# Kernel tuning notes

Measured on AMD Instinct MI355X. Metric: run time of the kernel, lower is better.

Reference implementation:

```python
import jax, jax.numpy as jnp
import numpy as np

B, S, N, H, C = 64, 512, 24, 768, 6

CONST_LAST = jnp.array([0.1, 0.1, 0.1, 0.3, 0.8, 0.01], dtype=jnp.float32)
CONST_MID = jnp.array([0.1, 0.1, 0.1, 0.8, 0.3, 0.01], dtype=jnp.float32)


def setup_inputs() -> dict:
    key = jax.random.key(0)
    k1, k2, k3, k4 = jax.random.split(key, 4)
    last_hidden_state = jax.random.normal(k1, (B, S, H), dtype=jnp.float32)
    # strictly increasing boundaries in [0, S-1]: sort randint in [0, S-N) then add arange(N)
    base = jnp.sort(jax.random.randint(k2, (B, N), 0, S - N), axis=1)
    sentence_token = base + jnp.arange(N, dtype=base.dtype)[None, :]
    W = jax.random.normal(k3, (C, H), dtype=jnp.float32) * 0.02
    b = jax.random.normal(k4, (C,), dtype=jnp.float32) * 0.02
    return {"last_hidden_state": last_hidden_state, "sentence_token": sentence_token,
            "W": W, "b": b}


def reference(last_hidden_state, sentence_token, W, b):
    # last_hidden_state: [B,S,H]; sentence_token: [B,N] strictly increasing boundaries.
    # Segment j covers tokens [prev+1, t_j] inclusive (prev = -1 for j==0).
    ends = sentence_token                                            # [B,N]
    prev = jnp.concatenate([-jnp.ones_like(ends[:, :1]), ends[:, :-1]], axis=1)
    # prefix sums with leading zero: csp[:, t+1] = sum of tokens 0..t
    cs = jnp.cumsum(last_hidden_state, axis=1)                       # [B,S,H]
    csp = jnp.concatenate([jnp.zeros_like(cs[:, :1]), cs], axis=1)   # [B,S+1,H]
    seg_sum = (jnp.take_along_axis(csp, (ends + 1)[:, :, None], axis=1)
               - jnp.take_along_axis(csp, (prev + 1)[:, :, None], axis=1))  # [B,N,H]
    lens = (ends - prev).astype(last_hidden_state.dtype)[:, :, None]  # >= 1 by construction
    seg_mean = seg_sum / lens                                         # [B,N,H]
    probs = jax.nn.sigmoid(jnp.einsum('bnh,ch->bnc', seg_mean, W) + b)  # [B,N,C]
    # override: boundary > 500 -> constant probability vector (different if last sentence)
    is_last = (jnp.arange(ends.shape[1]) == ends.shape[1] - 1)[None, :, None]  # [1,N,1]
    const = jnp.where(is_last, CONST_LAST[None, None, :], CONST_MID[None, None, :])
    over = (ends > 500)[:, :, None]
    return jnp.where(over, const, probs)
```

## Files before the change

### kernel.cpp

```cpp
#include <hip/hip_runtime.h>
#include <math.h>

#define B_ 64
#define S_ 512
#define N_ 24
#define H_ 768
#define C_ 6

__global__ __launch_bounds__(256) void proj_seg_kernel(
    const float* __restrict__ lhs, const int* __restrict__ st,
    const float* __restrict__ W, float* __restrict__ segsum, int ntok) {
  const int lane = threadIdx.x & 63;
  const int gwave = (int)((blockIdx.x * blockDim.x + threadIdx.x) >> 6);
  const int nwaves = (int)((gridDim.x * blockDim.x) >> 6);

  const float4* W4 = (const float4*)W;
  float4 w[3][C_];
#pragma unroll
  for (int k = 0; k < 3; ++k)
#pragma unroll
    for (int c = 0; c < C_; ++c)
      w[k][c] = W4[c * (H_ / 4) + k * 64 + lane];

  for (int t = gwave; t < ntok; t += nwaves) {
    const int b = t >> 9;
    const int s = t & 511;
    const int* stb = st + b * N_;
    if (s > stb[N_ - 1]) continue;

    int lo = 0, hi = N_ - 1;
    while (lo < hi) {
      int mid = (lo + hi) >> 1;
      if (stb[mid] < s) lo = mid + 1; else hi = mid;
    }

    const float4* x4 = (const float4*)(lhs + (size_t)t * H_);
    float acc[C_];
#pragma unroll
    for (int c = 0; c < C_; ++c) acc[c] = 0.0f;
#pragma unroll
    for (int k = 0; k < 3; ++k) {
      float4 x = x4[k * 64 + lane];
#pragma unroll
      for (int c = 0; c < C_; ++c)
        acc[c] += x.x * w[k][c].x + x.y * w[k][c].y +
                  x.z * w[k][c].z + x.w * w[k][c].w;
    }
#pragma unroll
    for (int c = 0; c < C_; ++c) {
      float v = acc[c];
      v += __shfl_down(v, 32, 64);
      v += __shfl_down(v, 16, 64);
      v += __shfl_down(v, 8, 64);
      v += __shfl_down(v, 4, 64);
      v += __shfl_down(v, 2, 64);
      v += __shfl_down(v, 1, 64);
      acc[c] = v;
    }
    if (lane == 0) {
      float* dst = segsum + ((size_t)b * N_ + lo) * C_;
#pragma unroll
      for (int c = 0; c < C_; ++c) atomicAdd(dst + c, acc[c]);
    }
  }
}

__global__ __launch_bounds__(256) void finalize_kernel(
    const float* __restrict__ segsum, const int* __restrict__ st,
    const float* __restrict__ bias, float* __restrict__ out) {
  int idx = blockIdx.x * blockDim.x + threadIdx.x;
  if (idx >= B_ * N_ * C_) return;
  int c = idx % C_;
  int j = (idx / C_) % N_;
  int b = idx / (N_ * C_);
  int end = st[b * N_ + j];
  int prev = (j == 0) ? -1 : st[b * N_ + j - 1];
  float len = (float)(end - prev);
  float logit = segsum[idx] / len + bias[c];
  float p = 1.0f / (1.0f + expf(-logit));
  if (end > 500) {
    float cl = (c < 3) ? 0.1f : (c == 3 ? 0.3f : (c == 4 ? 0.8f : 0.01f));
    float cm = (c < 3) ? 0.1f : (c == 3 ? 0.8f : (c == 4 ? 0.3f : 0.01f));
    p = (j == N_ - 1) ? cl : cm;
  }
  out[idx] = p;
}

extern "C" void kernel_launch(void* const* d_in, const int* in_sizes, int n_in,
                              void* d_out, int out_size, void* d_ws, size_t ws_size,
                              hipStream_t stream) {
  const float* lhs  = (const float*)d_in[0];
  const int*   st   = (const int*)d_in[1];
  const float* W    = (const float*)d_in[2];
  const float* bias = (const float*)d_in[3];
  float* segsum = (float*)d_ws;

  hipMemsetAsync(d_ws, 0, (size_t)B_ * N_ * C_ * sizeof(float), stream);
  proj_seg_kernel<<<2048, 256, 0, stream>>>(lhs, st, W, segsum, B_ * S_);
  finalize_kernel<<<(B_ * N_ * C_ + 255) / 256, 256, 0, stream>>>(
      segsum, st, bias, (float*)d_out);
}
```

Baseline: 183.7 us.

## Restructure segment projection into per-block LDS accumulators with chunked token tiles

Each block now owns a contiguous chunk of tokens for one batch and accumulates per-lane partial projections into a shared-memory array indexed by segment, class and lane. This replaces the per-token 6x6 shuffle reductions and global atomics. Segment lookup becomes a ballot/popcount over the boundaries held in registers instead of a binary search. Per-chunk partials go to workspace and are summed in the finalize kernel, with a fallback to global atomics when the workspace is too small. The costs are 36KB of LDS per block, LDS atomics, and extra finalize reads.

```diff
diff --git a/kernel.cpp b/kernel.cpp
--- a/kernel.cpp
+++ b/kernel.cpp
@@ -6,13 +6,40 @@
 #define N_ 24
 #define H_ 768
 #define C_ 6
+#define CHUNKS 16
+#define TOK_PER_BLOCK (S_ / CHUNKS)
+#define TOK_PER_WAVE (TOK_PER_BLOCK/4)
 
-__global__ __launch_bounds__(256) void proj_seg_kernel(
+__device__ __forceinline__ void do_token(const float4 x[3], const float4 w[3][C_],
+                                         int seg, int lane, float* acc) {
+  float a[C_];
+#pragma unroll
+  for (int c = 0; c < C_; ++c) a[c] = 0.f;
+#pragma unroll
+  for (int k = 0; k < 3; ++k)
+#pragma unroll
+    for (int c = 0; c < C_; ++c)
+      a[c] += x[k].x * w[k][c].x + x[k].y * w[k][c].y +
+              x[k].z * w[k][c].z + x[k].w * w[k][c].w;
+#pragma unroll
+  for (int c = 0; c < C_; ++c)
+    atomicAdd(&acc[(seg * C_ + c) * 64 + lane], a[c]);
+}
+
+__global__ __launch_bounds__(256, 4) void seg_proj_kernel(
     const float* __restrict__ lhs, const int* __restrict__ st,
-    const float* __restrict__ W, float* __restrict__ segsum, int ntok) {
-  const int lane = threadIdx.x & 63;
-  const int gwave = (int)((blockIdx.x * blockDim.x + threadIdx.x) >> 6);
-  const int nwaves = (int)((gridDim.x * blockDim.x) >> 6);
+    const float* __restrict__ W, float* __restrict__ outbuf, int use_atomic) {
+  __shared__ float acc[N_ * C_ * 64];
+  const int tid = threadIdx.x;
+  const int lane = tid & 63;
+  const int wave = tid >> 6;
+  const int b = blockIdx.x / CHUNKS;
+  const int chunk = blockIdx.x % CHUNKS;
+
+  for (int i = tid; i < N_ * C_ * 64; i += 256) acc[i] = 0.f;
+
+  int stb_l = st[b * N_ + (lane < N_ ? lane : N_ - 1)];
+  int last = __shfl(stb_l, N_ - 1, 64);
 
   const float4* W4 = (const float4*)W;
   float4 w[3][C_];
@@ -22,61 +49,66 @@
     for (int c = 0; c < C_; ++c)
       w[k][c] = W4[c * (H_ / 4) + k * 64 + lane];
 
-  for (int t = gwave; t < ntok; t += nwaves) {
-    const int b = t >> 9;
-    const int s = t & 511;
-    const int* stb = st + b * N_;
-    if (s > stb[N_ - 1]) continue;
+  __syncthreads();
 
-    int lo = 0, hi = N_ - 1;
-    while (lo < hi) {
-      int mid = (lo + hi) >> 1;
-      if (stb[mid] < s) lo = mid + 1; else hi = mid;
+  const int s_base = chunk * TOK_PER_BLOCK + wave * TOK_PER_WAVE;
+#pragma unroll
+  for (int g = 0; g < TOK_PER_WAVE / 2; ++g) {
+    const int s0 = s_base + g * 2;
+    const bool a0 = (s0 <= last);
+    const bool a1 = (s0 + 1 <= last);
+    const float4* x4 = (const float4*)(lhs + ((size_t)b * S_ + s0) * H_);
+    float4 x0[3], x1[3];
+    if (a0) {
+      x0[0] = x4[lane]; x0[1] = x4[64 + lane]; x0[2] = x4[128 + lane];
     }
+    if (a1) {
+      x1[0] = x4[192 + lane]; x1[1] = x4[256 + lane]; x1[2] = x4[320 + lane];
+    }
+    if (a0) {
+      unsigned long long m = __ballot(lane < N_ && stb_l < s0);
+      do_token(x0, w, (int)__popcll(m), lane, acc);
+    }
+    if (a1) {
+      unsigned long long m = __ballot(lane < N_ && stb_l < s0 + 1);
+      do_token(x1, w, (int)__popcll(m), lane, acc);
+    }
+  }
 
-    const float4* x4 = (const float4*)(lhs + (size_t)t * H_);
-    float acc[C_];
-#pragma unroll
-    for (int c = 0; c < C_; ++c) acc[c] = 0.0f;
-#pragma unroll
-    for (int k = 0; k < 3; ++k) {
-      float4 x = x4[k * 64 + lane];
-#pragma unroll
-      for (int c = 0; c < C_; ++c)
-        acc[c] += x.x * w[k][c].x + x.y * w[k][c].y +
-                  x.z * w[k][c].z + x.w * w[k][c].w;
-    }
-#pragma unroll
-    for (int c = 0; c < C_; ++c) {
-      float v = acc[c];
-      v += __shfl_down(v, 32, 64);
-      v += __shfl_down(v, 16, 64);
-      v += __shfl_down(v, 8, 64);
-      v += __shfl_down(v, 4, 64);
-      v += __shfl_down(v, 2, 64);
-      v += __shfl_down(v, 1, 64);
-      acc[c] = v;
-    }
-    if (lane == 0) {
-      float* dst = segsum + ((size_t)b * N_ + lo) * C_;
-#pragma unroll
-      for (int c = 0; c < C_; ++c) atomicAdd(dst + c, acc[c]);
-    }
+  __syncthreads();
+  if (tid < N_ * C_) {
+    float v = 0.f;
+    const int base = tid * 64;
+#pragma unroll 8
+    for (int i = 0; i < 64; ++i) v += acc[base + ((i + tid) & 63)];
+    if (use_atomic)
+      atomicAdd(&outbuf[b * N_ * C_ + tid], v);
+    else
+      outbuf[(size_t)blockIdx.x * (N_ * C_) + tid] = v;
   }
 }
 
 __global__ __launch_bounds__(256) void finalize_kernel(
-    const float* __restrict__ segsum, const int* __restrict__ st,
-    const float* __restrict__ bias, float* __restrict__ out) {
+    const float* __restrict__ buf, const int* __restrict__ st,
+    const float* __restrict__ bias, float* __restrict__ out, int use_atomic) {
   int idx = blockIdx.x * blockDim.x + threadIdx.x;
   if (idx >= B_ * N_ * C_) return;
   int c = idx % C_;
   int j = (idx / C_) % N_;
   int b = idx / (N_ * C_);
+  float ssum;
+  if (use_atomic) {
+    ssum = buf[idx];
+  } else {
+    ssum = 0.f;
+#pragma unroll
+    for (int k = 0; k < CHUNKS; ++k)
+      ssum += buf[(size_t)(b * CHUNKS + k) * (N_ * C_) + j * C_ + c];
+  }
   int end = st[b * N_ + j];
   int prev = (j == 0) ? -1 : st[b * N_ + j - 1];
   float len = (float)(end - prev);
-  float logit = segsum[idx] / len + bias[c];
+  float logit = ssum / len + bias[c];
   float p = 1.0f / (1.0f + expf(-logit));
   if (end > 500) {
     float cl = (c < 3) ? 0.1f : (c == 3 ? 0.3f : (c == 4 ? 0.8f : 0.01f));
@@ -93,10 +125,13 @@
   const int*   st   = (const int*)d_in[1];
   const float* W    = (const float*)d_in[2];
   const float* bias = (const float*)d_in[3];
-  float* segsum = (float*)d_ws;
 
-  hipMemsetAsync(d_ws, 0, (size_t)B_ * N_ * C_ * sizeof(float), stream);
-  proj_seg_kernel<<<2048, 256, 0, stream>>>(lhs, st, W, segsum, B_ * S_);
+  const size_t need = (size_t)B_ * CHUNKS * N_ * C_ * sizeof(float);
+  const int use_atomic = (ws_size < need) ? 1 : 0;
+  if (use_atomic)
+    hipMemsetAsync(d_ws, 0, (size_t)B_ * N_ * C_ * sizeof(float), stream);
+
+  seg_proj_kernel<<<B_ * CHUNKS, 256, 0, stream>>>(lhs, st, W, (float*)d_ws, use_atomic);
   finalize_kernel<<<(B_ * N_ * C_ + 255) / 256, 256, 0, stream>>>(
-      segsum, st, bias, (float*)d_out);
+      (float*)d_ws, st, bias, (float*)d_out, use_atomic);
 }
```

New measurement: 186.3 us. About the same (+1.4%).

## Project every token once, then reduce segments per batch in shared memory

Applied to the files above, without the earlier changes.

Computes a per-token projection onto the 6 classes and writes it to workspace instead of atomically accumulating segment sums. A per-batch finalize kernel loads those projections into shared memory and sums each segment directly. Each wave handles four tokens with batched loads, and uses DPP-based wave reductions. This removes the binary search, the atomics and the memset, but it now reads tokens past the last boundary.

```diff
diff --git a/kernel.cpp b/kernel.cpp
--- a/kernel.cpp
+++ b/kernel.cpp
@@ -7,12 +7,28 @@
 #define H_ 768
 #define C_ 6
 
-__global__ __launch_bounds__(256) void proj_seg_kernel(
-    const float* __restrict__ lhs, const int* __restrict__ st,
-    const float* __restrict__ W, float* __restrict__ segsum, int ntok) {
-  const int lane = threadIdx.x & 63;
-  const int gwave = (int)((blockIdx.x * blockDim.x + threadIdx.x) >> 6);
-  const int nwaves = (int)((gridDim.x * blockDim.x) >> 6);
+template <int CTRL>
+__device__ __forceinline__ float dpp_add(float v) {
+  int x = __builtin_amdgcn_update_dpp(0, __float_as_int(v), CTRL, 0xF, 0xF, true);
+  return v + __int_as_float(x);
+}
+__device__ __forceinline__ float wave_sum(float v) {
+  v = dpp_add<0xB1>(v);
+  v = dpp_add<0x4E>(v);
+  v = dpp_add<0x141>(v);
+  v = dpp_add<0x140>(v);
+  v += __shfl_xor(v, 16, 64);
+  v += __shfl_xor(v, 32, 64);
+  return v;
+}
+
+__global__ __launch_bounds__(256, 4) void proj_kernel(
+    const float* __restrict__ lhs, const float* __restrict__ W,
+    float* __restrict__ Y) {
+  const int tid = threadIdx.x;
+  const int lane = tid & 63;
+  const int gwave = (int)((blockIdx.x * 256 + tid) >> 6);
+  const int t_base = gwave * 4;
 
   const float4* W4 = (const float4*)W;
   float4 w[3][C_];
@@ -21,69 +37,84 @@
 #pragma unroll
     for (int c = 0; c < C_; ++c)
       w[k][c] = W4[c * (H_ / 4) + k * 64 + lane];
+#pragma unroll
+  for (int k = 0; k < 3; ++k)
+    asm volatile("" : "+v"(w[k][0].x), "+v"(w[k][0].y), "+v"(w[k][0].z), "+v"(w[k][0].w),
+                       "+v"(w[k][1].x), "+v"(w[k][1].y), "+v"(w[k][1].z), "+v"(w[k][1].w),
+                       "+v"(w[k][2].x), "+v"(w[k][2].y), "+v"(w[k][2].z), "+v"(w[k][2].w),
+                       "+v"(w[k][3].x), "+v"(w[k][3].y), "+v"(w[k][3].z), "+v"(w[k][3].w),
+                       "+v"(w[k][4].x), "+v"(w[k][4].y), "+v"(w[k][4].z), "+v"(w[k][4].w),
+                       "+v"(w[k][5].x), "+v"(w[k][5].y), "+v"(w[k][5].z), "+v"(w[k][5].w));
 
-  for (int t = gwave; t < ntok; t += nwaves) {
-    const int b = t >> 9;
-    const int s = t & 511;
-    const int* stb = st + b * N_;
-    if (s > stb[N_ - 1]) continue;
+  const float4* x4 = (const float4*)(lhs + (size_t)t_base * H_);
 
-    int lo = 0, hi = N_ - 1;
-    while (lo < hi) {
-      int mid = (lo + hi) >> 1;
-      if (stb[mid] < s) lo = mid + 1; else hi = mid;
-    }
+#pragma unroll
+  for (int r = 0; r < 2; ++r) {
+    float4 x0[3], x1[3];
+#pragma unroll
+    for (int k = 0; k < 3; ++k) x0[k] = x4[r * 384 + k * 64 + lane];
+#pragma unroll
+    for (int k = 0; k < 3; ++k) x1[k] = x4[r * 384 + 192 + k * 64 + lane];
 
-    const float4* x4 = (const float4*)(lhs + (size_t)t * H_);
-    float acc[C_];
 #pragma unroll
-    for (int c = 0; c < C_; ++c) acc[c] = 0.0f;
+    for (int tt = 0; tt < 2; ++tt) {
+      const float4* xx = tt ? x1 : x0;
+      float y[C_];
 #pragma unroll
-    for (int k = 0; k < 3; ++k) {
-      float4 x = x4[k * 64 + lane];
+      for (int c = 0; c < C_; ++c) y[c] = 0.f;
 #pragma unroll
-      for (int c = 0; c < C_; ++c)
-        acc[c] += x.x * w[k][c].x + x.y * w[k][c].y +
-                  x.z * w[k][c].z + x.w * w[k][c].w;
-    }
+      for (int k = 0; k < 3; ++k)
 #pragma unroll
-    for (int c = 0; c < C_; ++c) {
-      float v = acc[c];
-      v += __shfl_down(v, 32, 64);
-      v += __shfl_down(v, 16, 64);
-      v += __shfl_down(v, 8, 64);
-      v += __shfl_down(v, 4, 64);
-      v += __shfl_down(v, 2, 64);
-      v += __shfl_down(v, 1, 64);
-      acc[c] = v;
-    }
-    if (lane == 0) {
-      float* dst = segsum + ((size_t)b * N_ + lo) * C_;
+        for (int c = 0; c < C_; ++c)
+          y[c] += xx[k].x * w[k][c].x + xx[k].y * w[k][c].y +
+                  xx[k].z * w[k][c].z + xx[k].w * w[k][c].w;
 #pragma unroll
-      for (int c = 0; c < C_; ++c) atomicAdd(dst + c, acc[c]);
+      for (int c = 0; c < C_; ++c) y[c] = wave_sum(y[c]);
+      float out = y[0];
+      out = (lane == 1) ? y[1] : out;
+      out = (lane == 2) ? y[2] : out;
+      out = (lane == 3) ? y[3] : out;
+      out = (lane == 4) ? y[4] : out;
+      out = (lane == 5) ? y[5] : out;
+      const int t = t_base + r * 2 + tt;
+      if (lane < C_) Y[(size_t)t * C_ + lane] = out;
     }
   }
 }
 
-__global__ __launch_bounds__(256) void finalize_kernel(
-    const float* __restrict__ segsum, const int* __restrict__ st,
+__global__ __launch_bounds__(256) void seg_finalize(
+    const float* __restrict__ Y, const int* __restrict__ st,
     const float* __restrict__ bias, float* __restrict__ out) {
-  int idx = blockIdx.x * blockDim.x + threadIdx.x;
-  if (idx >= B_ * N_ * C_) return;
-  int c = idx % C_;
-  int j = (idx / C_) % N_;
-  int b = idx / (N_ * C_);
-  int end = st[b * N_ + j];
-  int prev = (j == 0) ? -1 : st[b * N_ + j - 1];
-  float len = (float)(end - prev);
-  float logit = segsum[idx] / len + bias[c];
-  float p = 1.0f / (1.0f + expf(-logit));
-  if (end > 500) {
-    float cl = (c < 3) ? 0.1f : (c == 3 ? 0.3f : (c == 4 ? 0.8f : 0.01f));
-    float cm = (c < 3) ? 0.1f : (c == 3 ? 0.8f : (c == 4 ? 0.3f : 0.01f));
-    p = (j == N_ - 1) ? cl : cm;
+  __shared__ float ly[S_ * C_];
+  __shared__ int lst[N_];
+  __shared__ float lb[C_];
+  const int tid = threadIdx.x;
+  const int b = blockIdx.x;
+
+  const float4* Y4 = (const float4*)(Y + (size_t)b * S_ * C_);
+  float4* ly4 = (float4*)ly;
+#pragma unroll
+  for (int i = 0; i < 3; ++i) ly4[i * 256 + tid] = Y4[i * 256 + tid];
+  if (tid < N_) lst[tid] = st[b * N_ + tid];
+  if (tid < C_) lb[tid] = bias[tid];
+  __syncthreads();
+
+  if (tid < N_ * C_) {
+    const int j = tid / C_;
+    const int c = tid % C_;
+    const int end = lst[j];
+    const int prev = (j == 0) ? -1 : lst[j - 1];
+    float s = 0.f;
+    for (int k = prev + 1; k <= end; ++k) s += ly[k * C_ + c];
+    float logit = s / (float)(end - prev) + lb[c];
+    float p = 1.0f / (1.0f + expf(-logit));
+    if (end > 500) {
+      float cl = (c < 3) ? 0.1f : (c == 3 ? 0.3f : (c == 4 ? 0.8f : 0.01f));
+      float cm = (c < 3) ? 0.1f : (c == 3 ? 0.8f : (c == 4 ? 0.3f : 0.01f));
+      p = (j == N_ - 1) ? cl : cm;
+    }
+    out[b * N_ * C_ + tid] = p;
   }
-  out[idx] = p;
 }
 
 extern "C" void kernel_launch(void* const* d_in, const int* in_sizes, int n_in,
@@ -93,10 +124,8 @@
   const int*   st   = (const int*)d_in[1];
   const float* W    = (const float*)d_in[2];
   const float* bias = (const float*)d_in[3];
-  float* segsum = (float*)d_ws;
+  float* Y = (float*)d_ws;
 
-  hipMemsetAsync(d_ws, 0, (size_t)B_ * N_ * C_ * sizeof(float), stream);
-  proj_seg_kernel<<<2048, 256, 0, stream>>>(lhs, st, W, segsum, B_ * S_);
-  finalize_kernel<<<(B_ * N_ * C_ + 255) / 256, 256, 0, stream>>>(
-      segsum, st, bias, (float*)d_out);
+  proj_kernel<<<2048, 256, 0, stream>>>(lhs, W, Y);
+  seg_finalize<<<B_, 256, 0, stream>>>(Y, st, bias, (float*)d_out);
 }
```

After: 157.4 us. 1.17x faster.
